# Performance work log

Measured on AMD Instinct MI355X. Metric: run time of the kernel, lower is better.

Reference implementation:

```python
import jax, jax.numpy as jnp
import numpy as np

ALPHA = 0.2  # LeakyReLU negative slope


def setup_inputs() -> dict:
    key = jax.random.key(0)
    k1, k2, k3, k4 = jax.random.split(key, 4)
    B, N, Fin, Fout = 8, 2048, 256, 256
    h = jax.random.normal(k1, (B, N, Fin), dtype=jnp.float32)
    # random 0/1 adjacency with guaranteed self-loops so every row has a neighbor
    adj = jax.random.randint(k2, (N, N), 0, 2).astype(jnp.float32)
    adj = jnp.maximum(adj, jnp.eye(N, dtype=jnp.float32))
    # xavier_uniform with gain=1.414
    def xavier(k, shape, gain=1.414):
        fan_in, fan_out = shape[0], shape[1]
        a = gain * np.sqrt(6.0 / (fan_in + fan_out))
        return jax.random.uniform(k, shape, dtype=jnp.float32, minval=-a, maxval=a)
    W = xavier(k3, (Fin, Fout))
    a = xavier(k4, (2 * Fout, 1))
    return {"h": h, "adj_matrix": adj, "W": W, "a": a}


def reference(h, adj_matrix, W, a):
    # h: [B, N, Fin], adj_matrix: [N, N], W: [Fin, Fout], a: [2*Fout, 1]
    Fout = W.shape[1]
    Wh = jnp.einsum("bnf,fo->bno", h, W)            # [B, N, Fout]
    a1, a2 = a[:Fout, 0], a[Fout:, 0]                 # split additive attention vector
    # e[b,i,j] = leakyrelu(Wh[b,i]@a1 + Wh[b,j]@a2) — equals concat([Wh_i,Wh_j])@a
    s1 = Wh @ a1                                      # [B, N]
    s2 = Wh @ a2                                      # [B, N]
    e = s1[:, :, None] + s2[:, None, :]               # [B, N, N]
    e = jnp.where(e >= 0, e, ALPHA * e)               # LeakyReLU
    e = jnp.where(adj_matrix[None] == 0, -jnp.inf, e)  # mask non-edges
    attention = jax.nn.softmax(e, axis=-1)            # [B, N, N]
    # dropout is identity in eval mode (training=False)
    h_prime = jnp.einsum("bij,bjo->bio", attention, Wh)
    return h_prime
```

## Files before the change

### kernel.cpp

```cpp
#include <hip/hip_runtime.h>
#include <cstdint>

#define NN 2048
#define LOG2E 1.4426950408889634f

typedef __attribute__((ext_vector_type(8))) short bf16x8;
typedef __attribute__((ext_vector_type(4))) float f32x4;

__device__ __forceinline__ unsigned short f2bf(float x){
  union { float f; unsigned u; } v; v.f = x;
  unsigned r = v.u + 0x7FFFu + ((v.u >> 16) & 1u);
  return (unsigned short)(r >> 16);
}
__device__ __forceinline__ unsigned pack2(float a, float b){
  return (unsigned)f2bf(a) | ((unsigned)f2bf(b) << 16);
}
__device__ __forceinline__ unsigned permpack(unsigned hi, unsigned lo){
  return __builtin_amdgcn_perm(hi, lo, 0x07060302u);
}

__global__ __launch_bounds__(256) void k_prep(const float* __restrict__ adj,
                                              const float* __restrict__ W,
                                              unsigned long long* __restrict__ ab,
                                              unsigned short* __restrict__ Wt){
  int tid = threadIdx.x;
  if (blockIdx.x < 2048){
    int i = blockIdx.x;
    int w = tid >> 6, lane = tid & 63;
    #pragma unroll
    for (int seg = 0; seg < 8; seg++){
      int j = seg * 256 + tid;
      unsigned long long m = __ballot(adj[(size_t)i * NN + j] != 0.0f);
      if (lane == 0) ab[i * 32 + seg * 4 + w] = m;
    }
  } else {
    int g = (blockIdx.x - 2048) * 256 + tid;
    int o = g >> 8, k = g & 255;
    Wt[g] = f2bf(W[k * 256 + o]);
  }
}

__global__ __launch_bounds__(256, 2) void k_fused_gemm(const float* __restrict__ h,
                                                       const unsigned short* __restrict__ Wt,
                                                       const float* __restrict__ a,
                                                       unsigned short* __restrict__ WhT,
                                                       float* __restrict__ s1c,
                                                       float* __restrict__ s2c){
  __shared__ __align__(16) unsigned short As[2][32 * 72];
  __shared__ __align__(16) unsigned short Ts[256 * 40];
  __shared__ float s1p[4][32], s2p[4][32];
  const int tid = threadIdx.x;
  const int r0 = blockIdx.x * 32;
  const int b  = r0 >> 11;
  const int i0 = r0 & (NN - 1);
  const int w = tid >> 6, lane = tid & 63, lhi = lane >> 4, llo = lane & 15;
  const int wc = w * 64;

  f32x4 acc[2][4];
  #pragma unroll
  for (int i = 0; i < 2; i++)
    #pragma unroll
    for (int j = 0; j < 4; j++){ acc[i][j][0]=0.f; acc[i][j][1]=0.f; acc[i][j][2]=0.f; acc[i][j][3]=0.f; }

  const int ar = tid >> 3;
  const int as_ = (tid & 7) * 8;

  float4 hv[4][2];
  #pragma unroll
  for (int t = 0; t < 4; t++){
    const float* hp = h + (size_t)(r0 + ar) * 256 + t * 64 + as_;
    hv[t][0] = *(const float4*)hp;
    hv[t][1] = *(const float4*)(hp + 4);
  }

  auto loadB = [&](int k0, bf16x8* dst){
    #pragma unroll
    for (int ot = 0; ot < 4; ot++)
      #pragma unroll
      for (int kk = 0; kk < 2; kk++)
        dst[ot * 2 + kk] = *(const bf16x8*)(Wt + (size_t)(wc + ot * 16 + llo) * 256 + k0 + kk * 32 + lhi * 8);
  };

  bf16x8 bfr[2][8];
  loadB(0, bfr[0]);

  #pragma unroll
  for (int t = 0; t < 4; t++){
    uint4 q = make_uint4(pack2(hv[t][0].x, hv[t][0].y), pack2(hv[t][0].z, hv[t][0].w),
                         pack2(hv[t][1].x, hv[t][1].y), pack2(hv[t][1].z, hv[t][1].w));
    if (t) __syncthreads();
    *(uint4*)&As[t & 1][ar * 72 + as_] = q;
    __syncthreads();
    if (t < 3) loadB((t + 1) * 64, bfr[(t + 1) & 1]);
    bf16x8 af[2][2];
    #pragma unroll
    for (int kk = 0; kk < 2; kk++)
      #pragma unroll
      for (int it = 0; it < 2; it++)
        af[kk][it] = *(const bf16x8*)&As[t & 1][(it * 16 + llo) * 72 + kk * 32 + lhi * 8];
    #pragma unroll
    for (int kk = 0; kk < 2; kk++)
      #pragma unroll
      for (int it = 0; it < 2; it++)
        #pragma unroll
        for (int ot = 0; ot < 4; ot++)
          acc[it][ot] = __builtin_amdgcn_mfma_f32_16x16x32_bf16(af[kk][it], bfr[t & 1][ot * 2 + kk], acc[it][ot], 0, 0, 0);
  }

  float a1v[4], a2v[4];
  #pragma unroll
  for (int ot = 0; ot < 4; ot++){
    a1v[ot] = a[wc + ot * 16 + llo] * LOG2E;
    a2v[ot] = a[256 + wc + ot * 16 + llo] * LOG2E;
  }
  #pragma unroll
  for (int it = 0; it < 2; it++){
    #pragma unroll
    for (int q = 0; q < 4; q++){
      float p1 = 0.f, p2 = 0.f;
      #pragma unroll
      for (int ot = 0; ot < 4; ot++){
        p1 += acc[it][ot][q] * a1v[ot];
        p2 += acc[it][ot][q] * a2v[ot];
      }
      #pragma unroll
      for (int o = 1; o < 16; o <<= 1){ p1 += __shfl_xor(p1, o); p2 += __shfl_xor(p2, o); }
      if (llo == 0){
        s1p[w][it * 16 + lhi * 4 + q] = p1;
        s2p[w][it * 16 + lhi * 4 + q] = p2;
      }
    }
  }

  #pragma unroll
  for (int it = 0; it < 2; it++){
    #pragma unroll
    for (int ot = 0; ot < 4; ot++){
      int o = wc + ot * 16 + llo;
      uint2 u = make_uint2(pack2(acc[it][ot][0], acc[it][ot][1]),
                           pack2(acc[it][ot][2], acc[it][ot][3]));
      *(uint2*)&Ts[o * 40 + it * 16 + lhi * 4] = u;
    }
  }
  __syncthreads();

  if (tid < 32){
    float t1 = 0.f, t2 = 0.f;
    #pragma unroll
    for (int g = 0; g < 4; g++){ t1 += s1p[g][tid]; t2 += s2p[g][tid]; }
    s1c[r0 + tid] = t1;
    s2c[r0 + tid] = t2;
  }
  #pragma unroll
  for (int p = 0; p < 4; p++){
    int o = p * 64 + (tid >> 2), col = (tid & 3) * 8;
    *(uint4*)(WhT + (size_t)(b * 256 + o) * 2048 + i0 + col) = *(const uint4*)&Ts[o * 40 + col];
  }
}

__global__ __launch_bounds__(256, 4) void k_attn(const float* __restrict__ s1c,
                                                 const float* __restrict__ s2c,
                                                 const unsigned short* __restrict__ WhT,
                                                 const unsigned long long* __restrict__ ab,
                                                 float* __restrict__ out){
  __shared__ __align__(16) float s2s[2048];
  __shared__ __align__(16) unsigned short Ps[2][32 * 72];
  __shared__ __align__(16) unsigned char bitsB[32 * 264];
  __shared__ float s1s[32], lin[32], red[4];
  const int tid = threadIdx.x;
  const int bid = blockIdx.x;
  const int b = bid & 7;
  const int r = bid >> 3;
  const int i0 = (r & 63) * 32;
  const int o0 = (r >> 6) * 128;
  const int w = tid >> 6, lane = tid & 63, lhi = lane >> 4, llo = lane & 15;
  const int co = o0 + w * 32;

  float4 v0 = ((const float4*)(s2c + (size_t)b * NN))[tid];
  float4 v1 = ((const float4*)(s2c + (size_t)b * NN))[tid + 256];
  ((float4*)s2s)[tid]       = v0;
  ((float4*)s2s)[tid + 256] = v1;
  float vmax = fmaxf(fmaxf(fmaxf(v0.x, v0.y), fmaxf(v0.z, v0.w)),
                     fmaxf(fmaxf(v1.x, v1.y), fmaxf(v1.z, v1.w)));
  #pragma unroll
  for (int o = 32; o; o >>= 1) vmax = fmaxf(vmax, __shfl_xor(vmax, o));
  if (lane == 0) red[w] = vmax;
  if (tid < 32) s1s[tid] = s1c[(size_t)b * NN + i0 + tid];
  #pragma unroll
  for (int k = 0; k < 4; k++){
    int g = k * 256 + tid;
    unsigned long long mw = ab[(size_t)i0 * 32 + g];
    *(unsigned long long*)&bitsB[(g >> 5) * 264 + (g & 31) * 8] = mw;
  }
  __syncthreads();
  float m2 = fmaxf(fmaxf(red[0], red[1]), fmaxf(red[2], red[3]));

  const int pi = tid >> 3;
  const int e8 = tid & 7;
  const int pj = e8 * 8;
  const float s1v = s1s[pi];
  const float xm = s1v + m2;
  const float mv = fmaxf(xm, 0.2f * xm);
  const float c1 = s1v - mv;
  const float c2 = 0.2f * s1v - mv;
  float rs = 0.f;

  f32x4 acc[2][2];
  #pragma unroll
  for (int i = 0; i < 2; i++)
    #pragma unroll
    for (int j = 0; j < 2; j++){ acc[i][j][0]=0.f; acc[i][j][1]=0.f; acc[i][j][2]=0.f; acc[i][j][3]=0.f; }

  auto loadB = [&](int j0, bf16x8* dst){
    #pragma unroll
    for (int ot = 0; ot < 2; ot++)
      #pragma unroll
      for (int kk = 0; kk < 2; kk++)
        dst[ot * 2 + kk] = *(const bf16x8*)(WhT + (size_t)(b * 256 + co + ot * 16 + llo) * 2048 + j0 + kk * 32 + lhi * 8);
  };

  unsigned pu[8];
  auto computeP = [&](int tn){
    unsigned bits = bitsB[pi * 264 + tn * 8 + e8];
    const float* sp = &s2s[tn * 64 + pj];
    float4 xa = *(const float4*)sp;
    float4 xb = *(const float4*)(sp + 4);
    float xs[8] = {xa.x, xa.y, xa.z, xa.w, xb.x, xb.y, xb.z, xb.w};
    #pragma unroll
    for (int e = 0; e < 8; e++){
      float s2v = xs[e];
      float y = fmaxf(s2v + c1, __builtin_fmaf(0.2f, s2v, c2));
      float p = __builtin_amdgcn_exp2f(y);
      unsigned m = ((bits >> e) & 1u) ? 0xFFFF0000u : 0u;
      unsigned u = __float_as_uint(p) & m;
      rs += __uint_as_float(u);
      pu[e] = u;
    }
  };

  auto stageBody = [&](int t, int BUF, bf16x8* curB, bf16x8* nxtB, bool last){
    uint4 q = make_uint4(permpack(pu[1], pu[0]), permpack(pu[3], pu[2]),
                         permpack(pu[5], pu[4]), permpack(pu[7], pu[6]));
    *(uint4*)&Ps[BUF][pi * 72 + pj] = q;
    __syncthreads();
    if (!last) loadB((t + 1) * 64, nxtB);
    bf16x8 af[2][2];
    #pragma unroll
    for (int kk = 0; kk < 2; kk++)
      #pragma unroll
      for (int it = 0; it < 2; it++)
        af[kk][it] = *(const bf16x8*)&Ps[BUF][(it * 16 + llo) * 72 + kk * 32 + lhi * 8];
    if (!last) computeP(t + 1);
    #pragma unroll
    for (int kk = 0; kk < 2; kk++)
      #pragma unroll
      for (int it = 0; it < 2; it++)
        #pragma unroll
        for (int ot = 0; ot < 2; ot++)
          acc[it][ot] = __builtin_amdgcn_mfma_f32_16x16x32_bf16(af[kk][it], curB[ot * 2 + kk], acc[it][ot], 0, 0, 0);
  };

  bf16x8 bA[4], bB[4];
  loadB(0, bA);
  computeP(0);
  for (int t2 = 0; t2 < 32; t2 += 2){
    stageBody(t2,     0, bA, bB, false);
    stageBody(t2 + 1, 1, bB, bA, t2 + 1 == 31);
  }

  rs += __shfl_xor(rs, 1);
  rs += __shfl_xor(rs, 2);
  rs += __shfl_xor(rs, 4);
  if (e8 == 0) lin[pi] = 1.0f / rs;
  __syncthreads();

  #pragma unroll
  for (int it = 0; it < 2; it++){
    #pragma unroll
    for (int ot = 0; ot < 2; ot++){
      int col = co + ot * 16 + llo;
      #pragma unroll
      for (int q = 0; q < 4; q++){
        int row = it * 16 + lhi * 4 + q;
        out[(size_t)(b * NN + i0 + row) * 256 + col] = acc[it][ot][q] * lin[row];
      }
    }
  }
}

extern "C" void kernel_launch(void* const* d_in, const int* in_sizes, int n_in,
                              void* d_out, int out_size, void* d_ws, size_t ws_size,
                              hipStream_t stream) {
  const float* h   = (const float*)d_in[0];
  const float* adj = (const float*)d_in[1];
  const float* W   = (const float*)d_in[2];
  const float* a   = (const float*)d_in[3];
  float* out = (float*)d_out;

  char* ws = (char*)d_ws;
  unsigned short* WhT      = (unsigned short*)(ws);
  unsigned short* Wt       = (unsigned short*)(ws + 8388608);
  unsigned long long* ab   = (unsigned long long*)(ws + 8519680);
  float* s1c               = (float*)(ws + 9043968);
  float* s2c               = (float*)(ws + 9109504);

  hipLaunchKernelGGL(k_prep,       dim3(2304), dim3(256), 0, stream, adj, W, ab, Wt);
  hipLaunchKernelGGL(k_fused_gemm, dim3(512),  dim3(256), 0, stream, h, Wt, a, WhT, s1c, s2c);
  hipLaunchKernelGGL(k_attn,       dim3(1024), dim3(256), 0, stream, s1c, s2c, WhT, ab, out);
}
```

Measured before the change: 157.1 us.

## Compute attention probabilities directly in MFMA A-fragments, drop LDS staging

The attention kernel now has each wave generate its own probability fragments in registers, in MFMA A-operand layout. This removes the shared-memory P buffer and the per-tile barriers. The row sums come from an extra MFMA against a ones vector, and each block now covers all 256 output columns with 8 accumulators, halving the grid to 512 blocks. The GEMM kernel also stores the h tile in fragment-linear LDS order and drops a barrier. The cost is more register pressure and duplicated exp work: each wave recomputes P for its 16 rows across both column halves. Occupancy is also lower, with launch bounds going from 4 to 2 blocks per CU.

```diff
diff --git a/kernel.cpp b/kernel.cpp
--- a/kernel.cpp
+++ b/kernel.cpp
@@ -46,15 +46,19 @@
                                                        unsigned short* __restrict__ WhT,
                                                        float* __restrict__ s1c,
                                                        float* __restrict__ s2c){
-  __shared__ __align__(16) unsigned short As[2][32 * 72];
-  __shared__ __align__(16) unsigned short Ts[256 * 40];
+  __shared__ __align__(16) unsigned char As[2 * 4096];
+  __shared__ __align__(16) unsigned short Ts[256 * 36];
   __shared__ float s1p[4][32], s2p[4][32];
   const int tid = threadIdx.x;
-  const int r0 = blockIdx.x * 32;
-  const int b  = r0 >> 11;
-  const int i0 = r0 & (NN - 1);
+  const int bid = blockIdx.x;
+  const int b  = bid & 7;
+  const int i0 = (bid >> 3) * 32;
+  const size_t r0 = (size_t)b * NN + i0;
   const int w = tid >> 6, lane = tid & 63, lhi = lane >> 4, llo = lane & 15;
   const int wc = w * 64;
+  const int sit = w & 1, skk = w >> 1;
+  const int srow = sit * 16 + llo;
+  const int skol = skk * 32 + lhi * 8;
 
   f32x4 acc[2][4];
   #pragma unroll
@@ -62,13 +66,10 @@
     #pragma unroll
     for (int j = 0; j < 4; j++){ acc[i][j][0]=0.f; acc[i][j][1]=0.f; acc[i][j][2]=0.f; acc[i][j][3]=0.f; }
 
-  const int ar = tid >> 3;
-  const int as_ = (tid & 7) * 8;
-
   float4 hv[4][2];
   #pragma unroll
   for (int t = 0; t < 4; t++){
-    const float* hp = h + (size_t)(r0 + ar) * 256 + t * 64 + as_;
+    const float* hp = h + (r0 + srow) * 256 + t * 64 + skol;
     hv[t][0] = *(const float4*)hp;
     hv[t][1] = *(const float4*)(hp + 4);
   }
@@ -80,7 +81,6 @@
       for (int kk = 0; kk < 2; kk++)
         dst[ot * 2 + kk] = *(const bf16x8*)(Wt + (size_t)(wc + ot * 16 + llo) * 256 + k0 + kk * 32 + lhi * 8);
   };
-
   bf16x8 bfr[2][8];
   loadB(0, bfr[0]);
 
@@ -88,8 +88,7 @@
   for (int t = 0; t < 4; t++){
     uint4 q = make_uint4(pack2(hv[t][0].x, hv[t][0].y), pack2(hv[t][0].z, hv[t][0].w),
                          pack2(hv[t][1].x, hv[t][1].y), pack2(hv[t][1].z, hv[t][1].w));
-    if (t) __syncthreads();
-    *(uint4*)&As[t & 1][ar * 72 + as_] = q;
+    *(uint4*)&As[(t & 1) * 4096 + (sit * 2 + skk) * 1024 + lane * 16] = q;
     __syncthreads();
     if (t < 3) loadB((t + 1) * 64, bfr[(t + 1) & 1]);
     bf16x8 af[2][2];
@@ -97,7 +96,7 @@
     for (int kk = 0; kk < 2; kk++)
       #pragma unroll
       for (int it = 0; it < 2; it++)
-        af[kk][it] = *(const bf16x8*)&As[t & 1][(it * 16 + llo) * 72 + kk * 32 + lhi * 8];
+        af[kk][it] = *(const bf16x8*)&As[(t & 1) * 4096 + (it * 2 + kk) * 1024 + lane * 16];
     #pragma unroll
     for (int kk = 0; kk < 2; kk++)
       #pragma unroll
@@ -139,7 +138,7 @@
       int o = wc + ot * 16 + llo;
       uint2 u = make_uint2(pack2(acc[it][ot][0], acc[it][ot][1]),
                            pack2(acc[it][ot][2], acc[it][ot][3]));
-      *(uint2*)&Ts[o * 40 + it * 16 + lhi * 4] = u;
+      *(uint2*)&Ts[o * 36 + it * 16 + lhi * 4] = u;
     }
   }
   __syncthreads();
@@ -154,27 +153,25 @@
   #pragma unroll
   for (int p = 0; p < 4; p++){
     int o = p * 64 + (tid >> 2), col = (tid & 3) * 8;
-    *(uint4*)(WhT + (size_t)(b * 256 + o) * 2048 + i0 + col) = *(const uint4*)&Ts[o * 40 + col];
-  }
-}
-
-__global__ __launch_bounds__(256, 4) void k_attn(const float* __restrict__ s1c,
+    *(uint4*)(WhT + (size_t)(b * 256 + o) * 2048 + i0 + col) = *(const uint4*)&Ts[o * 36 + col];
+  }
+}
+
+__global__ __launch_bounds__(256, 2) void k_attn(const float* __restrict__ s1c,
                                                  const float* __restrict__ s2c,
                                                  const unsigned short* __restrict__ WhT,
                                                  const unsigned long long* __restrict__ ab,
                                                  float* __restrict__ out){
   __shared__ __align__(16) float s2s[2048];
-  __shared__ __align__(16) unsigned short Ps[2][32 * 72];
   __shared__ __align__(16) unsigned char bitsB[32 * 264];
-  __shared__ float s1s[32], lin[32], red[4];
+  __shared__ float s1s[32], red[4];
   const int tid = threadIdx.x;
   const int bid = blockIdx.x;
-  const int b = bid & 7;
-  const int r = bid >> 3;
-  const int i0 = (r & 63) * 32;
-  const int o0 = (r >> 6) * 128;
+  const int b = bid & 7, i0 = (bid >> 3) * 32;
   const int w = tid >> 6, lane = tid & 63, lhi = lane >> 4, llo = lane & 15;
-  const int co = o0 + w * 32;
+  const int wi = w & 1, wo = w >> 1;
+  const int co = wo * 128;
+  const int prow = wi * 16 + llo;
 
   float4 v0 = ((const float4*)(s2c + (size_t)b * NN))[tid];
   float4 v1 = ((const float4*)(s2c + (size_t)b * NN))[tid + 256];
@@ -195,96 +192,64 @@
   __syncthreads();
   float m2 = fmaxf(fmaxf(red[0], red[1]), fmaxf(red[2], red[3]));
 
-  const int pi = tid >> 3;
-  const int e8 = tid & 7;
-  const int pj = e8 * 8;
-  const float s1v = s1s[pi];
+  const float s1v = s1s[prow];
   const float xm = s1v + m2;
   const float mv = fmaxf(xm, 0.2f * xm);
   const float c1 = s1v - mv;
   const float c2 = 0.2f * s1v - mv;
-  float rs = 0.f;
-
-  f32x4 acc[2][2];
-  #pragma unroll
-  for (int i = 0; i < 2; i++)
-    #pragma unroll
-    for (int j = 0; j < 2; j++){ acc[i][j][0]=0.f; acc[i][j][1]=0.f; acc[i][j][2]=0.f; acc[i][j][3]=0.f; }
-
-  auto loadB = [&](int j0, bf16x8* dst){
-    #pragma unroll
-    for (int ot = 0; ot < 2; ot++)
+
+  f32x4 acc[8], acc_l;
+  #pragma unroll
+  for (int j = 0; j < 8; j++){ acc[j][0]=0.f; acc[j][1]=0.f; acc[j][2]=0.f; acc[j][3]=0.f; }
+  acc_l[0]=0.f; acc_l[1]=0.f; acc_l[2]=0.f; acc_l[3]=0.f;
+
+  const uint4 onesq = make_uint4(0x3F803F80u, 0x3F803F80u, 0x3F803F80u, 0x3F803F80u);
+  const bf16x8 onesf = *(const bf16x8*)&onesq;
+
+  for (int t = 0; t < 32; t++){
+    bf16x8 bf[16];
+    #pragma unroll
+    for (int ot = 0; ot < 8; ot++)
       #pragma unroll
       for (int kk = 0; kk < 2; kk++)
-        dst[ot * 2 + kk] = *(const bf16x8*)(WhT + (size_t)(b * 256 + co + ot * 16 + llo) * 2048 + j0 + kk * 32 + lhi * 8);
-  };
-
-  unsigned pu[8];
-  auto computeP = [&](int tn){
-    unsigned bits = bitsB[pi * 264 + tn * 8 + e8];
-    const float* sp = &s2s[tn * 64 + pj];
-    float4 xa = *(const float4*)sp;
-    float4 xb = *(const float4*)(sp + 4);
-    float xs[8] = {xa.x, xa.y, xa.z, xa.w, xb.x, xb.y, xb.z, xb.w};
-    #pragma unroll
-    for (int e = 0; e < 8; e++){
-      float s2v = xs[e];
-      float y = fmaxf(s2v + c1, __builtin_fmaf(0.2f, s2v, c2));
-      float p = __builtin_amdgcn_exp2f(y);
-      unsigned m = ((bits >> e) & 1u) ? 0xFFFF0000u : 0u;
-      unsigned u = __float_as_uint(p) & m;
-      rs += __uint_as_float(u);
-      pu[e] = u;
-    }
-  };
-
-  auto stageBody = [&](int t, int BUF, bf16x8* curB, bf16x8* nxtB, bool last){
-    uint4 q = make_uint4(permpack(pu[1], pu[0]), permpack(pu[3], pu[2]),
-                         permpack(pu[5], pu[4]), permpack(pu[7], pu[6]));
-    *(uint4*)&Ps[BUF][pi * 72 + pj] = q;
-    __syncthreads();
-    if (!last) loadB((t + 1) * 64, nxtB);
-    bf16x8 af[2][2];
-    #pragma unroll
-    for (int kk = 0; kk < 2; kk++)
-      #pragma unroll
-      for (int it = 0; it < 2; it++)
-        af[kk][it] = *(const bf16x8*)&Ps[BUF][(it * 16 + llo) * 72 + kk * 32 + lhi * 8];
-    if (!last) computeP(t + 1);
-    #pragma unroll
-    for (int kk = 0; kk < 2; kk++)
-      #pragma unroll
-      for (int it = 0; it < 2; it++)
-        #pragma unroll
-        for (int ot = 0; ot < 2; ot++)
-          acc[it][ot] = __builtin_amdgcn_mfma_f32_16x16x32_bf16(af[kk][it], curB[ot * 2 + kk], acc[it][ot], 0, 0, 0);
-  };
-
-  bf16x8 bA[4], bB[4];
-  loadB(0, bA);
-  computeP(0);
-  for (int t2 = 0; t2 < 32; t2 += 2){
-    stageBody(t2,     0, bA, bB, false);
-    stageBody(t2 + 1, 1, bB, bA, t2 + 1 == 31);
-  }
-
-  rs += __shfl_xor(rs, 1);
-  rs += __shfl_xor(rs, 2);
-  rs += __shfl_xor(rs, 4);
-  if (e8 == 0) lin[pi] = 1.0f / rs;
-  __syncthreads();
-
-  #pragma unroll
-  for (int it = 0; it < 2; it++){
-    #pragma unroll
-    for (int ot = 0; ot < 2; ot++){
-      int col = co + ot * 16 + llo;
-      #pragma unroll
-      for (int q = 0; q < 4; q++){
-        int row = it * 16 + lhi * 4 + q;
-        out[(size_t)(b * NN + i0 + row) * 256 + col] = acc[it][ot][q] * lin[row];
+        bf[ot * 2 + kk] = *(const bf16x8*)(WhT + (size_t)(b * 256 + co + ot * 16 + llo) * 2048 + t * 64 + kk * 32 + lhi * 8);
+    bf16x8 af[2];
+    #pragma unroll
+    for (int kk = 0; kk < 2; kk++){
+      unsigned bits = bitsB[prow * 264 + t * 8 + kk * 4 + lhi];
+      const float* sp = &s2s[t * 64 + kk * 32 + lhi * 8];
+      float4 xa = *(const float4*)sp;
+      float4 xb = *(const float4*)(sp + 4);
+      float xs[8] = {xa.x, xa.y, xa.z, xa.w, xb.x, xb.y, xb.z, xb.w};
+      unsigned pu[8];
+      #pragma unroll
+      for (int e = 0; e < 8; e++){
+        float s2v = xs[e];
+        float y = fmaxf(s2v + c1, __builtin_fmaf(0.2f, s2v, c2));
+        float p = __builtin_amdgcn_exp2f(y);
+        unsigned msel = ((bits >> e) & 1u) ? 0xFFFF0000u : 0u;
+        pu[e] = __float_as_uint(p) & msel;
       }
-    }
+      uint4 q = make_uint4(permpack(pu[1], pu[0]), permpack(pu[3], pu[2]),
+                           permpack(pu[5], pu[4]), permpack(pu[7], pu[6]));
+      af[kk] = *(bf16x8*)&q;
+    }
+    #pragma unroll
+    for (int kk = 0; kk < 2; kk++){
+      acc_l = __builtin_amdgcn_mfma_f32_16x16x32_bf16(af[kk], onesf, acc_l, 0, 0, 0);
+      #pragma unroll
+      for (int ot = 0; ot < 8; ot++)
+        acc[ot] = __builtin_amdgcn_mfma_f32_16x16x32_bf16(af[kk], bf[ot * 2 + kk], acc[ot], 0, 0, 0);
+    }
+  }
+
+  #pragma unroll
+  for (int q = 0; q < 4; q++){
+    float lv = 1.0f / acc_l[q];
+    int row = i0 + wi * 16 + lhi * 4 + q;
+    #pragma unroll
+    for (int ot = 0; ot < 8; ot++)
+      out[(size_t)(b * NN + row) * 256 + co + ot * 16 + llo] = acc[ot][q] * lv;
   }
 }
 
@@ -306,5 +271,5 @@
 
   hipLaunchKernelGGL(k_prep,       dim3(2304), dim3(256), 0, stream, adj, W, ab, Wt);
   hipLaunchKernelGGL(k_fused_gemm, dim3(512),  dim3(256), 0, stream, h, Wt, a, WhT, s1c, s2c);
-  hipLaunchKernelGGL(k_attn,       dim3(1024), dim3(256), 0, stream, s1c, s2c, WhT, ab, out);
-}
+  hipLaunchKernelGGL(k_attn,       dim3(512),  dim3(256), 0, stream, s1c, s2c, WhT, ab, out);
+}
```

Result: slower. 211.1 us (+34.4%).
